# Optimization experiments

Measured on AMD Instinct MI355X. Metric: run time of the kernel, lower is better.

The kernel has to match this reference:

```python
import jax, jax.numpy as jnp
import numpy as np

EPS = 1e-5

def setup_inputs() -> dict:
    key = jax.random.key(0)
    kx, kw = jax.random.split(key)
    x = jax.random.normal(kx, (4, 2048, 4096), dtype=jnp.float32)
    W = jax.random.normal(kw, (4096, 4096), dtype=jnp.float32) * 0.02
    return {"x": x, "W": W}

def reference(x, W):
    # scale = mean absolute weight
    scale = jnp.mean(jnp.abs(W))
    Wn = W / (scale + EPS)
    # straight-through ternary rounding: forward = round(Wn), grad = identity
    Wq = Wn + jax.lax.stop_gradient(jnp.round(Wn) - Wn)
    # y = x @ Wq^T, then rescale by mean(|W|)
    y = jnp.einsum('bsi,oi->bso', x, Wq)
    return y * scale
```

## Files before the change

kernel.cpp:

```cpp
#include <hip/hip_runtime.h>


#define K_DIM 4096
#define N_DIM 4096
#define NKT   64

typedef __bf16 bf16x8 __attribute__((ext_vector_type(8)));
typedef float floatx4 __attribute__((ext_vector_type(4)));

__device__ __forceinline__ unsigned short f32_to_bf16(float f) {
    unsigned int u = __float_as_uint(f);
    u += 0x7fffu + ((u >> 16) & 1u);
    return (unsigned short)(u >> 16);
}

__global__ void reduce_abs_p1(const float4* __restrict__ W, double* __restrict__ partials, int n4) {
    int tid = blockIdx.x * blockDim.x + threadIdx.x;
    int stride = gridDim.x * blockDim.x;
    float s = 0.f;
    for (int i = tid; i < n4; i += stride) {
        float4 v = W[i];
        s += fabsf(v.x) + fabsf(v.y) + fabsf(v.z) + fabsf(v.w);
    }
    double d = (double)s;
#pragma unroll
    for (int o = 32; o > 0; o >>= 1) d += __shfl_down(d, o, 64);
    __shared__ double lds[4];
    if ((threadIdx.x & 63) == 0) lds[threadIdx.x >> 6] = d;
    __syncthreads();
    if (threadIdx.x == 0)
        partials[blockIdx.x] = lds[0] + lds[1] + lds[2] + lds[3];
}

__global__ void prep(const float4* __restrict__ W, const float4* __restrict__ X,
                     const double* __restrict__ partials, double* __restrict__ sum_out,
                     ushort4* __restrict__ Wq, ushort4* __restrict__ Xb,
                     int nW4, int nX4, double inv_cnt) {
    __shared__ double lds[4];
    double dsum;
    {
        int t = threadIdx.x;
        double d = partials[t] + partials[t + 256] + partials[t + 512] + partials[t + 768];
#pragma unroll
        for (int o = 32; o > 0; o >>= 1) d += __shfl_down(d, o, 64);
        if ((t & 63) == 0) lds[t >> 6] = d;
        __syncthreads();
        dsum = lds[0] + lds[1] + lds[2] + lds[3];
        if (blockIdx.x == 0 && t == 0) *sum_out = dsum;
    }
    float scale = (float)(dsum * inv_cnt);
    float d = scale + 1e-5f;
    int tid = blockIdx.x * blockDim.x + threadIdx.x;
    int stride = gridDim.x * blockDim.x;
    for (int i = tid; i < nW4; i += stride) {
        float4 v = W[i];
        ushort4 q;
        q.x = f32_to_bf16(rintf(v.x / d));
        q.y = f32_to_bf16(rintf(v.y / d));
        q.z = f32_to_bf16(rintf(v.z / d));
        q.w = f32_to_bf16(rintf(v.w / d));
        Wq[i] = q;
    }
    for (int i = tid; i < nX4; i += stride) {
        float4 v = X[i];
        ushort4 q;
        q.x = f32_to_bf16(v.x);
        q.y = f32_to_bf16(v.y);
        q.z = f32_to_bf16(v.z);
        q.w = f32_to_bf16(v.w);
        Xb[i] = q;
    }
}

__global__ __launch_bounds__(512, 2) void gemm_bt(
    const unsigned short* __restrict__ A, const unsigned short* __restrict__ B,
    float* __restrict__ C, const double* __restrict__ sum, double inv_cnt) {

    __shared__ __attribute__((aligned(16))) unsigned short As[2][2][128 * 64];
    __shared__ __attribute__((aligned(16))) unsigned short Bs[2][2][128 * 64];

    const int tid  = threadIdx.x;
    const int w    = tid >> 6;
    const int lane = tid & 63;
    const int wm   = w >> 2;
    const int wn   = w & 3;

    const int bid = blockIdx.y * gridDim.x + blockIdx.x;
    const int swz = (bid & 7) * 64 + (bid >> 3);
    const size_t m0 = (size_t)(swz >> 4) * 256;
    const size_t n0 = (size_t)(swz & 15) * 256;

    const int srow   = lane >> 3;
    const int schunk = (lane & 7) ^ srow;
    const unsigned short* pA = A + (m0 + (size_t)(w * 8 + srow)) * K_DIM + schunk * 8;
    const unsigned short* pB = B + (n0 + (size_t)(w * 8 + srow)) * K_DIM + schunk * 8;

    const int fm    = lane & 15;
    const int q     = lane >> 4;
    const int cs0   = (q ^ (fm & 7)) * 8;
    const int cs1   = ((4 + q) ^ (fm & 7)) * 8;
    const int abase = fm * 64;
    const int bh    = wn >> 1;
    const int bbase = (wn & 1) * 4096 + fm * 64;

    floatx4 acc[8][4] = {};
    bf16x8 a0[2][4];
    bf16x8 a1[2][4];
    bf16x8 Be[2][2];
    bf16x8 Bo[2][2];

#define STAGE_A(bb, h, kt) do {                                                            \
        __builtin_amdgcn_global_load_lds(                                                  \
            (const __attribute__((address_space(1))) void*)(pA + ((h) * 128 + 0) * K_DIM + (kt) * 64), \
            (__attribute__((address_space(3))) void*)&As[bb][h][w * 512 + 0], 16, 0, 0);   \
        __builtin_amdgcn_global_load_lds(                                                  \
            (const __attribute__((address_space(1))) void*)(pA + ((h) * 128 + 64) * K_DIM + (kt) * 64), \
            (__attribute__((address_space(3))) void*)&As[bb][h][w * 512 + 4096], 16, 0, 0); \
    } while (0)

#define STAGE_B(bb, h, kt) do {                                                            \
        __builtin_amdgcn_global_load_lds(                                                  \
            (const __attribute__((address_space(1))) void*)(pB + ((h) * 128 + 0) * K_DIM + (kt) * 64), \
            (__attribute__((address_space(3))) void*)&Bs[bb][h][w * 512 + 0], 16, 0, 0);   \
        __builtin_amdgcn_global_load_lds(                                                  \
            (const __attribute__((address_space(1))) void*)(pB + ((h) * 128 + 64) * K_DIM + (kt) * 64), \
            (__attribute__((address_space(3))) void*)&Bs[bb][h][w * 512 + 4096], 16, 0, 0); \
    } while (0)

#define READ_A_HALF(dst, b, mh) do {                                                       \
        _Pragma("unroll")                                                                  \
        for (int t = 0; t < 4; ++t) {                                                      \
            dst[0][t] = *(const bf16x8*)&As[b][wm][((mh) * 4 + t) * 1024 + abase + cs0];   \
            dst[1][t] = *(const bf16x8*)&As[b][wm][((mh) * 4 + t) * 1024 + abase + cs1];   \
        }                                                                                  \
    } while (0)

#define READ_B_HALF(dst, b, nh) do {                                                       \
        _Pragma("unroll")                                                                  \
        for (int u = 0; u < 2; ++u) {                                                      \
            dst[0][u] = *(const bf16x8*)&Bs[b][bh][bbase + ((nh) * 2 + u) * 1024 + cs0];   \
            dst[1][u] = *(const bf16x8*)&Bs[b][bh][bbase + ((nh) * 2 + u) * 1024 + cs1];   \
        }                                                                                  \
    } while (0)

#define MFMA16(mh, nh, Af, Bf) do {                                                        \
        _Pragma("unroll")                                                                  \
        for (int ks = 0; ks < 2; ++ks)                                                     \
            _Pragma("unroll")                                                              \
            for (int t = 0; t < 4; ++t)                                                    \
                _Pragma("unroll")                                                          \
                for (int u = 0; u < 2; ++u)                                                \
                    acc[(mh) * 4 + t][(nh) * 2 + u] = __builtin_amdgcn_mfma_f32_16x16x32_bf16( \
                        Af[ks][t], Bf[ks][u], acc[(mh) * 4 + t][(nh) * 2 + u], 0, 0, 0);   \
    } while (0)

#define KTILE(b, j, P, Q, DOA, DOB, PFB, PFA, VM1S, VM2S) do {                             \
                                 \
        READ_B_HALF(Q, b, 1);                                                              \
        if (DOA) STAGE_A((b) ^ 1, 0, (j) + 1);                                             \
        __builtin_amdgcn_s_barrier();                                                      \
        __builtin_amdgcn_s_setprio(1);                                                     \
        MFMA16(0, 0, a0, P);                                                               \
        __builtin_amdgcn_s_setprio(0);                                                     \
        __builtin_amdgcn_s_barrier();                                                      \
                                    \
        READ_A_HALF(a1, b, 1);                                                             \
        if (DOA) STAGE_A((b) ^ 1, 1, (j) + 1);                                             \
        __builtin_amdgcn_s_barrier();                                                      \
        __builtin_amdgcn_s_setprio(1);                                                     \
        MFMA16(0, 1, a0, Q);                                                               \
        __builtin_amdgcn_s_setprio(0);                                                     \
        asm volatile(VM1S ::: "memory");                                                   \
        __builtin_amdgcn_s_barrier();                                                      \
                          \
        if (DOB) STAGE_B(b, 0, (j) + 2);                                                   \
        __builtin_amdgcn_s_barrier();                                                      \
        __builtin_amdgcn_s_setprio(1);                                                     \
        MFMA16(1, 1, a1, Q);                                                               \
        __builtin_amdgcn_s_setprio(0);                                                     \
        if (PFB) READ_B_HALF(Q, (b) ^ 1, 0);                                               \
        asm volatile(VM2S ::: "memory");                                                   \
        __builtin_amdgcn_s_barrier();                                                      \
                              \
        if (PFA) READ_A_HALF(a0, (b) ^ 1, 0);                                              \
        if (DOB) STAGE_B(b, 1, (j) + 2);                                                   \
        __builtin_amdgcn_s_barrier();                                                      \
        __builtin_amdgcn_s_setprio(1);                                                     \
        MFMA16(1, 0, a1, P);                                                               \
        __builtin_amdgcn_s_setprio(0);                                                     \
        __builtin_amdgcn_s_barrier();                                                      \
    } while (0)

    STAGE_A(0, 0, 0); STAGE_A(0, 1, 0);
    STAGE_B(0, 0, 0); STAGE_B(0, 1, 0);
    STAGE_B(1, 0, 1); STAGE_B(1, 1, 1);
    asm volatile("s_waitcnt vmcnt(4)" ::: "memory");
    __builtin_amdgcn_s_barrier();
    READ_A_HALF(a0, 0, 0);
    READ_B_HALF(Be, 0, 0);

    for (int j = 0; j < NKT - 2; j += 2) {
        KTILE(0, j,     Be, Bo, 1, 1, 1, 1, "s_waitcnt vmcnt(4)", "s_waitcnt vmcnt(2)");
        KTILE(1, j + 1, Bo, Be, 1, 1, 1, 1, "s_waitcnt vmcnt(4)", "s_waitcnt vmcnt(2)");
    }
    KTILE(0, NKT - 2, Be, Bo, 1, 0, 1, 1, "s_waitcnt vmcnt(4)", "s_waitcnt vmcnt(0)");
    KTILE(1, NKT - 1, Bo, Be, 0, 0, 0, 0, "", "");

#undef KTILE
#undef MFMA16
#undef READ_B_HALF
#undef READ_A_HALF
#undef STAGE_B
#undef STAGE_A

    const float scale = (float)(*sum * inv_cnt);
    const size_t m0c = m0 + (size_t)wm * 128;
    const size_t n0c = n0 + (size_t)wn * 64;
#pragma unroll
    for (int mf = 0; mf < 8; ++mf) {
#pragma unroll
        for (int nf = 0; nf < 4; ++nf) {
            float* cp = C + (m0c + mf * 16 + q * 4) * N_DIM + n0c + nf * 16 + fm;
#pragma unroll
            for (int r = 0; r < 4; ++r)
                cp[(size_t)r * N_DIM] = acc[mf][nf][r] * scale;
        }
    }
}

extern "C" void kernel_launch(void* const* d_in, const int* in_sizes, int n_in,
                              void* d_out, int out_size, void* d_ws, size_t ws_size,
                              hipStream_t stream) {
    const float* x = (const float*)d_in[0];
    const float* W = (const float*)d_in[1];
    float* y = (float*)d_out;

    const int nW = in_sizes[1];
    const int M  = in_sizes[0] / K_DIM;

    double* d_sum = (double*)d_ws;
    double* d_partials = (double*)((char*)d_ws + 16);
    unsigned short* xb = (unsigned short*)((char*)d_ws + 16 + 1024 * sizeof(double));
    unsigned short* wq = xb + (size_t)M * K_DIM;
    const double inv_cnt = 1.0 / (double)nW;

    reduce_abs_p1<<<1024, 256, 0, stream>>>((const float4*)W, d_partials, nW / 4);
    prep<<<2048, 256, 0, stream>>>((const float4*)W, (const float4*)x, d_partials, d_sum,
                                   (ushort4*)wq, (ushort4*)xb,
                                   nW / 4, in_sizes[0] / 4, inv_cnt);

    dim3 grid(N_DIM / 256, M / 256);
    gemm_bt<<<grid, 512, 0, stream>>>(xb, wq, y, d_sum, inv_cnt);
}
```

Baseline: 578.6 us.

## Switch GEMM inner loop to 32x32x16 bf16 MFMA with new LDS fragment schedule

Replaces the 16x16x32 MFMA tiling with 32x32x16 bf16 MFMA instructions, so each wave holds 4x2 floatx16 accumulators. LDS fragment reads are restructured to match the 32-row layout, and the per-k-tile schedule now loads A/B fragments just in time with explicit lgkmcnt waits instead of prefetching the next tile's fragments. The larger MFMA shape is meant to cut LDS read traffic and instruction count per FLOP. In exchange, cross-tile fragment prefetch is lost, which may expose LDS latency, and the output store pattern changes.

```diff
diff --git a/kernel.cpp b/kernel.cpp
--- a/kernel.cpp
+++ b/kernel.cpp
@@ -6,7 +6,7 @@
 #define NKT   64
 
 typedef __bf16 bf16x8 __attribute__((ext_vector_type(8)));
-typedef float floatx4 __attribute__((ext_vector_type(4)));
+typedef float floatx16 __attribute__((ext_vector_type(16)));
 
 __device__ __forceinline__ unsigned short f32_to_bf16(float f) {
     unsigned int u = __float_as_uint(f);
@@ -95,19 +95,20 @@
     const unsigned short* pA = A + (m0 + (size_t)(w * 8 + srow)) * K_DIM + schunk * 8;
     const unsigned short* pB = B + (n0 + (size_t)(w * 8 + srow)) * K_DIM + schunk * 8;
 
-    const int fm    = lane & 15;
-    const int q     = lane >> 4;
-    const int cs0   = (q ^ (fm & 7)) * 8;
-    const int cs1   = ((4 + q) ^ (fm & 7)) * 8;
-    const int abase = fm * 64;
+    const int r31   = lane & 31;
+    const int hk    = lane >> 5;
+    const int xor7  = r31 & 7;
+    const int abase = r31 * 64;
     const int bh    = wn >> 1;
-    const int bbase = (wn & 1) * 4096 + fm * 64;
-
-    floatx4 acc[8][4] = {};
-    bf16x8 a0[2][4];
-    bf16x8 a1[2][4];
-    bf16x8 Be[2][2];
-    bf16x8 Bo[2][2];
+    const int bbase = ((wn & 1) * 64 + r31) * 64;
+
+#define CHK(ks) ((((ks) * 2 + hk) ^ xor7) * 8)
+
+    floatx16 acc[4][2] = {};
+    bf16x8 a0f[2][4];
+    bf16x8 a1f[2][4];
+    bf16x8 b0f[4];
+    bf16x8 b1f[4];
 
 #define STAGE_A(bb, h, kt) do {                                                            \
         __builtin_amdgcn_global_load_lds(                                                  \
@@ -129,101 +130,103 @@
 
 #define READ_A_HALF(dst, b, mh) do {                                                       \
         _Pragma("unroll")                                                                  \
-        for (int t = 0; t < 4; ++t) {                                                      \
-            dst[0][t] = *(const bf16x8*)&As[b][wm][((mh) * 4 + t) * 1024 + abase + cs0];   \
-            dst[1][t] = *(const bf16x8*)&As[b][wm][((mh) * 4 + t) * 1024 + abase + cs1];   \
-        }                                                                                  \
-    } while (0)
-
-#define READ_B_HALF(dst, b, nh) do {                                                       \
+        for (int mfl = 0; mfl < 2; ++mfl)                                                  \
+            _Pragma("unroll")                                                              \
+            for (int ks = 0; ks < 4; ++ks)                                                 \
+                dst[mfl][ks] = *(const bf16x8*)                                            \
+                    &As[b][wm][((mh) * 2 + mfl) * 2048 + abase + CHK(ks)];                 \
+    } while (0)
+
+#define READ_B_NF(dst, b, nf) do {                                                         \
         _Pragma("unroll")                                                                  \
-        for (int u = 0; u < 2; ++u) {                                                      \
-            dst[0][u] = *(const bf16x8*)&Bs[b][bh][bbase + ((nh) * 2 + u) * 1024 + cs0];   \
-            dst[1][u] = *(const bf16x8*)&Bs[b][bh][bbase + ((nh) * 2 + u) * 1024 + cs1];   \
-        }                                                                                  \
-    } while (0)
-
-#define MFMA16(mh, nh, Af, Bf) do {                                                        \
+        for (int ks = 0; ks < 4; ++ks)                                                     \
+            dst[ks] = *(const bf16x8*)                                                     \
+                &Bs[b][bh][bbase + (nf) * 2048 + CHK(ks)];                                 \
+    } while (0)
+
+#define MFMA8(mh, nf, Af, Bf) do {                                                         \
         _Pragma("unroll")                                                                  \
-        for (int ks = 0; ks < 2; ++ks)                                                     \
+        for (int ks = 0; ks < 4; ++ks)                                                     \
             _Pragma("unroll")                                                              \
-            for (int t = 0; t < 4; ++t)                                                    \
-                _Pragma("unroll")                                                          \
-                for (int u = 0; u < 2; ++u)                                                \
-                    acc[(mh) * 4 + t][(nh) * 2 + u] = __builtin_amdgcn_mfma_f32_16x16x32_bf16( \
-                        Af[ks][t], Bf[ks][u], acc[(mh) * 4 + t][(nh) * 2 + u], 0, 0, 0);   \
-    } while (0)
-
-#define KTILE(b, j, P, Q, DOA, DOB, PFB, PFA, VM1S, VM2S) do {                             \
-                                 \
-        READ_B_HALF(Q, b, 1);                                                              \
+            for (int mfl = 0; mfl < 2; ++mfl)                                              \
+                acc[(mh) * 2 + mfl][nf] = __builtin_amdgcn_mfma_f32_32x32x16_bf16(         \
+                    Af[mfl][ks], Bf[ks], acc[(mh) * 2 + mfl][nf], 0, 0, 0);                \
+    } while (0)
+
+#define KTILE(b, j, DOA, DOB, VMW) do {                                                    \
+                                                                                   \
+        READ_A_HALF(a0f, b, 0);                                                            \
+        READ_B_NF(b0f, b, 0);                                                              \
         if (DOA) STAGE_A((b) ^ 1, 0, (j) + 1);                                             \
-        __builtin_amdgcn_s_barrier();                                                      \
-        __builtin_amdgcn_s_setprio(1);                                                     \
-        MFMA16(0, 0, a0, P);                                                               \
-        __builtin_amdgcn_s_setprio(0);                                                     \
-        __builtin_amdgcn_s_barrier();                                                      \
-                                    \
-        READ_A_HALF(a1, b, 1);                                                             \
+        asm volatile("s_waitcnt lgkmcnt(8)" ::: "memory");                                 \
+        __builtin_amdgcn_s_barrier();                                                      \
+        asm volatile("s_waitcnt lgkmcnt(0)" ::: "memory");                                 \
+        __builtin_amdgcn_s_setprio(1);                                                     \
+        MFMA8(0, 0, a0f, b0f);                                                             \
+        __builtin_amdgcn_s_setprio(0);                                                     \
+        __builtin_amdgcn_s_barrier();                                                      \
+                                                                                   \
+        READ_B_NF(b1f, b, 1);                                                              \
         if (DOA) STAGE_A((b) ^ 1, 1, (j) + 1);                                             \
         __builtin_amdgcn_s_barrier();                                                      \
-        __builtin_amdgcn_s_setprio(1);                                                     \
-        MFMA16(0, 1, a0, Q);                                                               \
-        __builtin_amdgcn_s_setprio(0);                                                     \
-        asm volatile(VM1S ::: "memory");                                                   \
-        __builtin_amdgcn_s_barrier();                                                      \
-                          \
+        asm volatile("s_waitcnt lgkmcnt(0)" ::: "memory");                                 \
+        __builtin_amdgcn_s_setprio(1);                                                     \
+        MFMA8(0, 1, a0f, b1f);                                                             \
+        __builtin_amdgcn_s_setprio(0);                                                     \
+        __builtin_amdgcn_s_barrier();                                                      \
+                                                                                   \
+        READ_A_HALF(a1f, b, 1);                                                            \
         if (DOB) STAGE_B(b, 0, (j) + 2);                                                   \
         __builtin_amdgcn_s_barrier();                                                      \
-        __builtin_amdgcn_s_setprio(1);                                                     \
-        MFMA16(1, 1, a1, Q);                                                               \
-        __builtin_amdgcn_s_setprio(0);                                                     \
-        if (PFB) READ_B_HALF(Q, (b) ^ 1, 0);                                               \
-        asm volatile(VM2S ::: "memory");                                                   \
-        __builtin_amdgcn_s_barrier();                                                      \
-                              \
-        if (PFA) READ_A_HALF(a0, (b) ^ 1, 0);                                              \
+        asm volatile("s_waitcnt lgkmcnt(0)" ::: "memory");                                 \
+        __builtin_amdgcn_s_setprio(1);                                                     \
+        MFMA8(1, 0, a1f, b0f);                                                             \
+        __builtin_amdgcn_s_setprio(0);                                                     \
+        __builtin_amdgcn_s_barrier();                                                      \
+                                                                                   \
         if (DOB) STAGE_B(b, 1, (j) + 2);                                                   \
         __builtin_amdgcn_s_barrier();                                                      \
         __builtin_amdgcn_s_setprio(1);                                                     \
-        MFMA16(1, 0, a1, P);                                                               \
-        __builtin_amdgcn_s_setprio(0);                                                     \
-        __builtin_amdgcn_s_barrier();                                                      \
-    } while (0)
-
+        MFMA8(1, 1, a1f, b1f);                                                             \
+        __builtin_amdgcn_s_setprio(0);                                                     \
+        asm volatile(VMW ::: "memory");                                                    \
+        __builtin_amdgcn_s_barrier();                                                      \
+    } while (0)
+
+    STAGE_B(0, 0, 0); STAGE_B(0, 1, 0);
     STAGE_A(0, 0, 0); STAGE_A(0, 1, 0);
-    STAGE_B(0, 0, 0); STAGE_B(0, 1, 0);
     STAGE_B(1, 0, 1); STAGE_B(1, 1, 1);
     asm volatile("s_waitcnt vmcnt(4)" ::: "memory");
     __builtin_amdgcn_s_barrier();
-    READ_A_HALF(a0, 0, 0);
-    READ_B_HALF(Be, 0, 0);
 
     for (int j = 0; j < NKT - 2; j += 2) {
-        KTILE(0, j,     Be, Bo, 1, 1, 1, 1, "s_waitcnt vmcnt(4)", "s_waitcnt vmcnt(2)");
-        KTILE(1, j + 1, Bo, Be, 1, 1, 1, 1, "s_waitcnt vmcnt(4)", "s_waitcnt vmcnt(2)");
-    }
-    KTILE(0, NKT - 2, Be, Bo, 1, 0, 1, 1, "s_waitcnt vmcnt(4)", "s_waitcnt vmcnt(0)");
-    KTILE(1, NKT - 1, Bo, Be, 0, 0, 0, 0, "", "");
+        KTILE(0, j,     1, 1, "s_waitcnt vmcnt(4)");
+        KTILE(1, j + 1, 1, 1, "s_waitcnt vmcnt(4)");
+    }
+    KTILE(0, NKT - 2, 1, 0, "s_waitcnt vmcnt(0)");
+    KTILE(1, NKT - 1, 0, 0, "");
 
 #undef KTILE
-#undef MFMA16
-#undef READ_B_HALF
+#undef MFMA8
+#undef READ_B_NF
 #undef READ_A_HALF
 #undef STAGE_B
 #undef STAGE_A
+#undef CHK
 
     const float scale = (float)(*sum * inv_cnt);
     const size_t m0c = m0 + (size_t)wm * 128;
     const size_t n0c = n0 + (size_t)wn * 64;
 #pragma unroll
-    for (int mf = 0; mf < 8; ++mf) {
-#pragma unroll
-        for (int nf = 0; nf < 4; ++nf) {
-            float* cp = C + (m0c + mf * 16 + q * 4) * N_DIM + n0c + nf * 16 + fm;
-#pragma unroll
-            for (int r = 0; r < 4; ++r)
-                cp[(size_t)r * N_DIM] = acc[mf][nf][r] * scale;
+    for (int mf = 0; mf < 4; ++mf) {
+#pragma unroll
+        for (int nf = 0; nf < 2; ++nf) {
+#pragma unroll
+            for (int r = 0; r < 16; ++r) {
+                size_t row = m0c + mf * 32 + (r & 3) + 8 * (r >> 2) + 4 * hk;
+                size_t col = n0c + nf * 32 + r31;
+                C[row * N_DIM + col] = acc[mf][nf][r] * scale;
+            }
         }
     }
 }
```

Measured after the change: 575.2 us. No clear change (-0.6%).
